# Kernel optimization log

Measured on AMD Instinct MI355X. Metric: run time of the kernel, lower is better.

## Reference

```python
import jax, jax.numpy as jnp
import numpy as np
from jax import lax

TAU = 2.0          # spikingjelly LIFNode default tau
VTH = 1.0          # v_threshold
ALPHA = 2.0        # ATan surrogate alpha (grad only; fwd is heaviside)
N_WIN = (2, 4, 4)
TOPK = 4
HEADS = 8
EPS = 1e-5


@jax.custom_vjp
def spike(x):
    return (x >= 0).astype(x.dtype)

def _spike_fwd(x):
    return (x >= 0).astype(x.dtype), x

def _spike_bwd(x, g):
    sg = (ALPHA / 2.0) / (1.0 + (jnp.pi / 2.0 * ALPHA * x) ** 2)
    return (g * sg,)

spike.defvjp(_spike_fwd, _spike_bwd)


def lif(x_seq):
    # multi-step LIF, v_reset=None (soft reset), decay_input=True, detach_reset
    def step(v, x):
        v = v + (x - v) / TAU
        s = spike(v - VTH)
        v = v - lax.stop_gradient(s) * VTH
        return v, s
    v0 = jnp.zeros_like(x_seq[0])
    _, s_seq = lax.scan(step, v0, x_seq)
    return s_seq


def bn3d(x, g, b):
    # track_running_stats=False -> always batch stats; step_mode 'm' folds T into batch.
    # x: [T,B,C,Lt,Lh,Lw]; normalize per-channel over (T,B,Lt,Lh,Lw)
    ax = (0, 1, 3, 4, 5)
    m = x.mean(ax, keepdims=True)
    v = x.var(ax, keepdims=True)
    sh = (1, 1, -1, 1, 1, 1)
    return g.reshape(sh) * (x - m) * lax.rsqrt(v + EPS) + b.reshape(sh)


def bra(x, wqkv, bqkv, lepe_w, wo, bo):
    # Bi-level routing attention over 3D windows. x: [N, Lt, Lh, Lw, C]
    N, Lt, Lh, Lw, C = x.shape
    nt, nh, nw = N_WIN
    rt, rh, rw = Lt // nt, Lh // nh, Lw // nw
    R, P = nt * nh * nw, rt * rh * rw
    Dh = C // HEADS

    qkv = x @ wqkv + bqkv                       # [N,Lt,Lh,Lw,3C]
    q, k, v = jnp.split(qkv, 3, axis=-1)

    def to_reg(t):  # -> [N, R, P, C]
        t = t.reshape(N, nt, rt, nh, rh, nw, rw, C)
        return t.transpose(0, 1, 3, 5, 2, 4, 6, 7).reshape(N, R, P, C)

    def from_reg(t):  # [N,R,P,C] -> [N,Lt,Lh,Lw,C]
        t = t.reshape(N, nt, nh, nw, rt, rh, rw, C)
        return t.transpose(0, 1, 4, 2, 5, 3, 6, 7).reshape(N, Lt, Lh, Lw, C)

    qr, kr, vr = to_reg(q), to_reg(k), to_reg(v)

    # coarse routing: region means, top-k region selection
    a_r = jnp.einsum('nrc,nsc->nrs', qr.mean(2), kr.mean(2))   # [N,R,R]
    _, idx = lax.top_k(a_r, TOPK)                               # [N,R,TOPK]

    # gather selected regions' k,v: [N,R,TOPK,P,C] -> [N,R,TOPK*P,H,Dh]
    kg = jax.vmap(lambda a, i: a[i])(kr, idx)
    vg = jax.vmap(lambda a, i: a[i])(vr, idx)
    kg = kg.reshape(N, R, TOPK * P, HEADS, Dh)
    vg = vg.reshape(N, R, TOPK * P, HEADS, Dh)
    qh = qr.reshape(N, R, P, HEADS, Dh)

    logits = jnp.einsum('nrphd,nrkhd->nrhpk', qh * (Dh ** -0.5), kg)
    attn = jax.nn.softmax(logits, axis=-1)
    out = jnp.einsum('nrhpk,nrkhd->nrphd', attn, vg).reshape(N, R, P, C)
    out = from_reg(out)

    # LEPE: depthwise 3x3x3 conv on v
    v_ncdhw = v.transpose(0, 4, 1, 2, 3)
    lepe = lax.conv_general_dilated(
        v_ncdhw, lepe_w, (1, 1, 1), 'SAME', feature_group_count=C,
        dimension_numbers=('NCDHW', 'OIDHW', 'NCDHW'))
    out = out + lepe.transpose(0, 2, 3, 4, 1)

    return out @ wo + bo


def setup_inputs() -> dict:
    key = jax.random.key(0)
    ks = jax.random.split(key, 8)
    T, B, C, Lt, Lh, Lw = 2, 1, 256, 8, 32, 32
    inp = {
        'x': jax.random.normal(ks[0], (T, B, C, Lt, Lh, Lw), jnp.float32),
        'bn1_g': jnp.ones((C,), jnp.float32),
        'bn1_b': jnp.zeros((C,), jnp.float32),
        'wqkv': jax.random.normal(ks[1], (C, 3 * C), jnp.float32) * (C ** -0.5),
        'bqkv': jnp.zeros((3 * C,), jnp.float32),
        'lepe_w': jax.random.normal(ks[2], (C, 1, 3, 3, 3), jnp.float32) * 0.1,
        'wo': jax.random.normal(ks[3], (C, C), jnp.float32) * (C ** -0.5),
        'bo': jnp.zeros((C,), jnp.float32),
        'bn2_g': jnp.ones((C,), jnp.float32),
        'bn2_b': jnp.zeros((C,), jnp.float32),
        'ffn_w1': jax.random.normal(ks[4], (C, 4 * C), jnp.float32) * (C ** -0.5),
        'ffn_b1': jnp.zeros((4 * C,), jnp.float32),
        'ffn_w2': jax.random.normal(ks[5], (4 * C, C), jnp.float32) * ((4 * C) ** -0.5),
        'ffn_b2': jnp.zeros((C,), jnp.float32),
        'scale': jnp.ones((1,), jnp.float32) * 0.5,
    }
    return inp


def reference(x, bn1_g, bn1_b, wqkv, bqkv, lepe_w, wo, bo,
              bn2_g, bn2_b, ffn_w1, ffn_b1, ffn_w2, ffn_b2, scale):
    T, B, C, Lt, Lh, Lw = x.shape

    # --- attention branch ---
    s1 = lif(bn3d(x, bn1_g, bn1_b))                       # [T,B,C,Lt,Lh,Lw]
    sa = s1.transpose(0, 1, 3, 4, 5, 2).reshape(T * B, Lt, Lh, Lw, C)
    a = bra(sa, wqkv, bqkv, lepe_w, wo, bo)
    a = a.reshape(T, B, Lt, Lh, Lw, C).transpose(0, 1, 5, 2, 3, 4)
    x = x + a * scale

    # --- FFN branch (1x1x1 conv = channel GEMM) ---
    s2 = lif(bn3d(x, bn2_g, bn2_b))
    h = jax.nn.gelu(jnp.einsum('tbcdhw,cf->tbfdhw', s2, ffn_w1)
                    + ffn_b1.reshape(1, 1, -1, 1, 1, 1), approximate=False)
    f = (jnp.einsum('tbfdhw,fc->tbcdhw', h, ffn_w2)
         + ffn_b2.reshape(1, 1, -1, 1, 1, 1))
    return x + f * scale
```

## Files before the change

kernel.cpp:

```cpp
#include <hip/hip_runtime.h>
#include <math.h>

#define CC 256
#define LL 8192
#define RR 32
#define PPP 256
#define NTOP 4
#define TOKS 16384
#define TBLK (TOKS * 32)

typedef unsigned short u16;
typedef __attribute__((ext_vector_type(8))) short short8;
typedef __attribute__((ext_vector_type(8))) unsigned short u16x8;
typedef __attribute__((ext_vector_type(4))) float f32x4;
typedef __attribute__((ext_vector_type(4))) unsigned short u16x4;

#if defined(__has_builtin)
#if __has_builtin(__builtin_amdgcn_exp2f)
#define EXP2(x) __builtin_amdgcn_exp2f(x)
#endif
#endif
#ifndef EXP2
#define EXP2(x) exp2f(x)
#endif

__device__ inline u16 f2bf(float f) {
  unsigned int b = __float_as_uint(f);
  unsigned int r = (b + 0x7FFFu + ((b >> 16) & 1u)) >> 16;
  return (u16)r;
}
__device__ inline float bf2f(u16 x) { return __uint_as_float(((unsigned int)x) << 16); }

__global__ __launch_bounds__(256) void k_bnstats(const float* __restrict__ x,
                                                 float* __restrict__ mean,
                                                 float* __restrict__ istd) {
  int c = blockIdx.x, tid = threadIdx.x;
  float s = 0.f, sq = 0.f;
  for (int i = tid; i < 2 * LL / 4; i += 256) {
    int t = i >> 11, l4 = (i & 2047) * 4;
    float4 v = *(const float4*)&x[(size_t)(t * CC + c) * LL + l4];
    s += (v.x + v.y) + (v.z + v.w);
    sq += (v.x * v.x + v.y * v.y) + (v.z * v.z + v.w * v.w);
  }
  __shared__ float rs[256], rq[256];
  rs[tid] = s; rq[tid] = sq;
  __syncthreads();
  for (int off = 128; off > 0; off >>= 1) {
    if (tid < off) { rs[tid] += rs[tid + off]; rq[tid] += rq[tid + off]; }
    __syncthreads();
  }
  if (tid == 0) {
    float m = rs[0] * (1.f / (2 * LL));
    float var = rq[0] * (1.f / (2 * LL)) - m * m;
    mean[c] = m;
    istd[c] = rsqrtf(var + 1e-5f);
  }
}

__global__ __launch_bounds__(128) void k_bnfin(const float* __restrict__ psum,
                                               const float* __restrict__ psq,
                                               float* __restrict__ mean,
                                               float* __restrict__ istd) {
  int c = blockIdx.x;
  int tid = threadIdx.x;
  __shared__ float rs[128], rq[128];
  rs[tid] = psum[c * 128 + tid];
  rq[tid] = psq[c * 128 + tid];
  __syncthreads();
  for (int off = 64; off > 0; off >>= 1) {
    if (tid < off) { rs[tid] += rs[tid + off]; rq[tid] += rq[tid + off]; }
    __syncthreads();
  }
  if (tid == 0) {
    float m = rs[0] * (1.f / 16384.f);
    float var = rq[0] * (1.f / 16384.f) - m * m;
    mean[c] = m;
    istd[c] = rsqrtf(var + 1e-5f);
  }
}

__global__ __launch_bounds__(256) void k_lifT(const float* __restrict__ xin,
                                              const float* __restrict__ mean,
                                              const float* __restrict__ istd,
                                              const float* __restrict__ g,
                                              const float* __restrict__ b,
                                              u16* __restrict__ actT) {
  __shared__ float t0[32][33], t1[32][33];
  int l0 = blockIdx.x * 32, c0 = blockIdx.y * 32;
  int tx = threadIdx.x & 31, ty = threadIdx.x >> 5;
  for (int i = 0; i < 32; i += 8) {
    int c = c0 + ty + i;
    float m = mean[c], is = istd[c], gg = g[c], bb = b[c];
    float x0 = xin[(size_t)c * LL + l0 + tx];
    float x1 = xin[(size_t)(CC + c) * LL + l0 + tx];
    float y0 = gg * (x0 - m) * is + bb;
    float y1 = gg * (x1 - m) * is + bb;
    float v = y0 * 0.5f;
    float s0 = (v >= 1.f) ? 1.f : 0.f;
    v -= s0;
    v += (y1 - v) * 0.5f;
    float s1 = (v >= 1.f) ? 1.f : 0.f;
    t0[ty + i][tx] = s0;
    t1[ty + i][tx] = s1;
  }
  __syncthreads();
  size_t kb = (size_t)(c0 >> 5) * TBLK;
  for (int i = 0; i < 32; i += 8) {
    int l = l0 + ty + i;
    actT[kb + (size_t)l * 32 + tx] = f2bf(t0[tx][ty + i]);
    actT[kb + (size_t)(LL + l) * 32 + tx] = f2bf(t1[tx][ty + i]);
  }
}

__device__ inline void tr_tile(const float* __restrict__ in, u16* __restrict__ out,
                               int C, int c0, int r0) {
  __shared__ float t[32][33];
  int tx = threadIdx.x & 31, ty = threadIdx.x >> 5;
  for (int i = 0; i < 32; i += 8)
    t[ty + i][tx] = in[(size_t)(r0 + ty + i) * C + c0 + tx];
  __syncthreads();
  size_t kb = (size_t)(r0 >> 5) * C * 32;
  for (int i = 0; i < 32; i += 8)
    out[kb + (size_t)(c0 + ty + i) * 32 + tx] = f2bf(t[tx][ty + i]);
}

__global__ __launch_bounds__(256) void k_trall(const float* __restrict__ wqkv,
                                               const float* __restrict__ w1,
                                               const float* __restrict__ w2,
                                               const float* __restrict__ wo,
                                               const float* __restrict__ lep,
                                               u16* __restrict__ wqkvT, u16* __restrict__ w1T,
                                               u16* __restrict__ w2T, u16* __restrict__ woT,
                                               float* __restrict__ wTlep) {
  int b = blockIdx.x;
  if (b < 192) {
    tr_tile(wqkv, wqkvT, 768, (b % 24) * 32, (b / 24) * 32);
  } else if (b < 448) {
    int i = b - 192;
    tr_tile(w1, w1T, 1024, (i % 32) * 32, (i / 32) * 32);
  } else if (b < 704) {
    int i = b - 448;
    tr_tile(w2, w2T, 256, (i % 8) * 32, (i / 8) * 32);
  } else if (b < 768) {
    int i = b - 704;
    tr_tile(wo, woT, 256, (i % 8) * 32, (i / 8) * 32);
  } else {
    int c = threadIdx.x;
    for (int tap = 0; tap < 27; ++tap) wTlep[tap * 256 + c] = lep[c * 27 + tap];
  }
}

template<int MR, int NR, int KTOT>
__device__ inline void mfma_core_w(const u16* __restrict__ A0, int sAb,
                                   const u16* __restrict__ B0, int sBb,
                                   int wr, int wc, f32x4 acc[MR][NR]) {
  int lane = threadIdx.x & 63;
  int u = lane & 15;
  int g8 = (lane >> 4) * 8;
  const u16* Ap = A0 + (wr * MR * 16 + u) * 32 + g8;
  const u16* Bp = B0 + (wc * NR * 16 + u) * 32 + g8;
  constexpr int NKB = KTOT >> 5;
  short8 aA[MR], bA[NR], aB[MR], bB[NR];
#pragma unroll
  for (int i = 0; i < MR; ++i) aA[i] = *(const short8*)(Ap + i * 512);
#pragma unroll
  for (int j = 0; j < NR; ++j) bA[j] = *(const short8*)(Bp + j * 512);
#pragma unroll
  for (int kb = 0; kb < NKB; kb += 2) {
    if (kb + 1 < NKB) {
#pragma unroll
      for (int i = 0; i < MR; ++i) aB[i] = *(const short8*)(Ap + (size_t)(kb + 1) * sAb + i * 512);
#pragma unroll
      for (int j = 0; j < NR; ++j) bB[j] = *(const short8*)(Bp + (size_t)(kb + 1) * sBb + j * 512);
    }
#pragma unroll
    for (int i = 0; i < MR; ++i)
#pragma unroll
      for (int j = 0; j < NR; ++j)
        acc[i][j] = __builtin_amdgcn_mfma_f32_16x16x32_bf16(aA[i], bA[j], acc[i][j], 0, 0, 0);
    if (kb + 2 < NKB) {
#pragma unroll
      for (int i = 0; i < MR; ++i) aA[i] = *(const short8*)(Ap + (size_t)(kb + 2) * sAb + i * 512);
#pragma unroll
      for (int j = 0; j < NR; ++j) bA[j] = *(const short8*)(Bp + (size_t)(kb + 2) * sBb + j * 512);
    }
    if (kb + 1 < NKB) {
#pragma unroll
      for (int i = 0; i < MR; ++i)
#pragma unroll
        for (int j = 0; j < NR; ++j)
          acc[i][j] = __builtin_amdgcn_mfma_f32_16x16x32_bf16(aB[i], bB[j], acc[i][j], 0, 0, 0);
    }
  }
}

__global__ __launch_bounds__(256) void k_gqkv(const u16* __restrict__ spkT, const u16* __restrict__ wT,
                                              const float* __restrict__ bias,
                                              u16* __restrict__ qh, u16* __restrict__ kh,
                                              u16* __restrict__ vt, u16* __restrict__ vtok) {
  f32x4 acc[4][4] = {};
  int m0 = blockIdx.x * 128, n0 = blockIdx.y * 128;
  int w = threadIdx.x >> 6;
  mfma_core_w<4, 4, 256>(spkT + (size_t)m0 * 32, TBLK, wT + (size_t)n0 * 32, 768 * 32,
                         w >> 1, w & 1, acc);
  int lane = threadIdx.x & 63;
  int wr = w >> 1, wc = w & 1;
  int u = lane & 15;
  const float QSC = 0.255034865f;
#pragma unroll
  for (int i = 0; i < 4; ++i) {
    int token0 = m0 + wr * 64 + i * 16 + (lane >> 4) * 4;
    int l = token0 & (LL - 1), nb = token0 >> 13;
    int lt = l >> 10, lh = (l >> 5) & 31, lw = l & 31;
    int r = ((lt >> 2) * 4 + (lh >> 3)) * 4 + (lw >> 3);
    int p0 = ((lt & 3) * 8 + (lh & 7)) * 8 + (lw & 7);
    int nr = nb * RR + r;
#pragma unroll
    for (int j = 0; j < 4; ++j) {
      int ch = n0 + wc * 64 + j * 16 + u;
      int which = ch >> 8, c = ch & 255;
      int hh = c >> 5, dh = c & 31;
      size_t hb = ((size_t)nr * 8 + hh) * 8192;
      float bb = bias[ch];
      if (which == 0) {
#pragma unroll
        for (int reg = 0; reg < 4; ++reg)
          qh[hb + (p0 + reg) * 32 + dh] = f2bf((acc[i][j][reg] + bb) * QSC);
      } else if (which == 1) {
#pragma unroll
        for (int reg = 0; reg < 4; ++reg)
          kh[hb + (p0 + reg) * 32 + dh] = f2bf(acc[i][j][reg] + bb);
      } else {
        u16x4 pk;
#pragma unroll
        for (int reg = 0; reg < 4; ++reg) {
          u16 vb = f2bf(acc[i][j][reg] + bb);
          pk[reg] = vb;
          vtok[(size_t)(token0 + reg) * CC + c] = vb;
        }
        *(u16x4*)&vt[hb + dh * 256 + p0] = pk;
      }
    }
  }
}

__global__ __launch_bounds__(256) void k_means(const u16* __restrict__ qh, const u16* __restrict__ kh,
                                               float* __restrict__ qm, float* __restrict__ km) {
  int nrh = blockIdx.x;
  int nr = nrh >> 3, h = nrh & 7;
  int tid = threadIdx.x;
  int dh = tid & 31, pg = tid >> 5;
  size_t base = (size_t)nrh * 8192;
  float sq = 0.f, sk = 0.f;
  for (int p = pg * 32; p < pg * 32 + 32; ++p) {
    sq += bf2f(qh[base + p * 32 + dh]);
    sk += bf2f(kh[base + p * 32 + dh]);
  }
  __shared__ float rq[256], rk[256];
  rq[tid] = sq; rk[tid] = sk;
  __syncthreads();
  if (pg == 0) {
#pragma unroll
    for (int g = 1; g < 8; ++g) { sq += rq[g * 32 + dh]; sk += rk[g * 32 + dh]; }
    qm[nr * 256 + h * 32 + dh] = sq * (1.f / 256);
    km[nr * 256 + h * 32 + dh] = sk * (1.f / 256);
  }
}

__global__ __launch_bounds__(256) void k_route(const float* __restrict__ qm,
                                               const float* __restrict__ km,
                                               int* __restrict__ idx) {
  int nr = blockIdx.x;
  int n = nr >> 5;
  int tid = threadIdx.x;
  int s = tid >> 3, cg = tid & 7;
  const float* qrow = qm + nr * CC;
  const float* krow = km + (n * RR + s) * CC;
  float sum = 0.f;
  for (int c = cg * 32; c < cg * 32 + 32; ++c) sum += qrow[c] * krow[c];
  sum += __shfl_xor(sum, 1);
  sum += __shfl_xor(sum, 2);
  sum += __shfl_xor(sum, 4);
  __shared__ float ar[32];
  if (cg == 0) ar[s] = sum;
  __syncthreads();
  if (tid == 0) {
    for (int t = 0; t < NTOP; ++t) {
      float best = -1e30f; int bi = 0;
      for (int ss = 0; ss < 32; ++ss)
        if (ar[ss] > best) { best = ar[ss]; bi = ss; }
      ar[bi] = -1e30f;
      idx[nr * NTOP + t] = bi;
    }
  }
}

__global__ __launch_bounds__(256) void k_attn_mfma(const u16* __restrict__ qh,
                                                   const u16* __restrict__ kh,
                                                   const u16* __restrict__ vt,
                                                   const int* __restrict__ idx,
                                                   u16* __restrict__ oreg) {
  int h = blockIdx.x, r = blockIdx.y, n = blockIdx.z;
  int nr = n * RR + r;
  int lane = threadIdx.x & 63;
  int w = threadIdx.x >> 6;
  int u = lane & 15, g = lane >> 4;
  int swz = (u >> 1) & 3;
  __shared__ __align__(16) unsigned pl[4096];
  unsigned* plw = &pl[w * 1024];

  const u16* qb = qh + ((size_t)nr * 8 + h) * 8192;
  int q0 = w * 64;
  short8 qf[4];
#pragma unroll
  for (int f = 0; f < 4; ++f)
    qf[f] = *(const short8*)(qb + (size_t)(q0 + f * 16 + u) * 32 + g * 8);

  f32x4 accO[2][4] = {};
  float lsum[4] = {0.f, 0.f, 0.f, 0.f};
  const int* idxp = &idx[nr * NTOP];

  for (int ri = 0; ri < NTOP; ++ri) {
    int reg = idxp[ri];
    size_t rb = ((size_t)(n * RR + reg) * 8 + h) * 8192;
#pragma unroll 2
    for (int t = 0; t < 8; ++t) {
      int pb = t * 32;
      short8 kf0 = *(const short8*)(kh + rb + (size_t)(pb + u) * 32 + g * 8);
      short8 kf1 = *(const short8*)(kh + rb + (size_t)(pb + 16 + u) * 32 + g * 8);
      short8 vf0 = *(const short8*)(vt + rb + (size_t)u * 256 + pb + g * 8);
      short8 vf1 = *(const short8*)(vt + rb + (size_t)(16 + u) * 256 + pb + g * 8);

      f32x4 s0[4], s1[4];
      __builtin_amdgcn_s_setprio(1);
#pragma unroll
      for (int nf = 0; nf < 4; ++nf) {
        s0[nf] = __builtin_amdgcn_mfma_f32_16x16x32_bf16(kf0, qf[nf], (f32x4){0.f, 0.f, 0.f, 0.f}, 0, 0, 0);
        s1[nf] = __builtin_amdgcn_mfma_f32_16x16x32_bf16(kf1, qf[nf], (f32x4){0.f, 0.f, 0.f, 0.f}, 0, 0, 0);
      }
      __builtin_amdgcn_s_setprio(0);
#pragma unroll
      for (int nf = 0; nf < 4; ++nf) {
#pragma unroll
        for (int mf = 0; mf < 2; ++mf) {
          f32x4 sv = mf ? s1[nf] : s0[nf];
          float p0 = EXP2(sv[0]);
          float p1 = EXP2(sv[1]);
          float p2 = EXP2(sv[2]);
          float p3 = EXP2(sv[3]);
          lsum[nf] += (p0 + p1) + (p2 + p3);
          unsigned wA, wB;
          asm("v_cvt_pk_bf16_f32 %0, %1, %2" : "=v"(wA) : "v"(p0), "v"(p1));
          asm("v_cvt_pk_bf16_f32 %0, %1, %2" : "=v"(wB) : "v"(p2), "v"(p3));
          int bidx = (mf * 2 + (g >> 1)) ^ swz;
          *(uint2*)&plw[nf * 256 + u * 16 + bidx * 4 + (g & 1) * 2] = make_uint2(wA, wB);
        }
      }
      __builtin_amdgcn_s_setprio(1);
#pragma unroll
      for (int nf = 0; nf < 4; ++nf) {
        short8 pf = *(const short8*)&plw[nf * 256 + u * 16 + ((g ^ swz) << 2)];
        accO[0][nf] = __builtin_amdgcn_mfma_f32_16x16x32_bf16(vf0, pf, accO[0][nf], 0, 0, 0);
        accO[1][nf] = __builtin_amdgcn_mfma_f32_16x16x32_bf16(vf1, pf, accO[1][nf], 0, 0, 0);
      }
      __builtin_amdgcn_s_setprio(0);
    }
  }

#pragma unroll
  for (int nf = 0; nf < 4; ++nf) {
    lsum[nf] += __shfl_xor(lsum[nf], 16);
    lsum[nf] += __shfl_xor(lsum[nf], 32);
    float inv = 1.f / lsum[nf];
    int q = q0 + nf * 16 + u;
    int z = (((r >> 4) & 1) << 2) | ((q >> 6) & 3);
    int y = (((r >> 2) & 3) << 3) | ((q >> 3) & 7);
    int xx = ((r & 3) << 3) | (q & 7);
    int l = (z << 10) | (y << 5) | xx;
    u16* ob = &oreg[((size_t)(n * LL + l)) * CC + h * 32];
#pragma unroll
    for (int mf = 0; mf < 2; ++mf) {
      f32x4 o = mf ? accO[1][nf] : accO[0][nf];
      float a0 = o[0] * inv, a1 = o[1] * inv, a2 = o[2] * inv, a3 = o[3] * inv;
      unsigned w0, w1;
      asm("v_cvt_pk_bf16_f32 %0, %1, %2" : "=v"(w0) : "v"(a0), "v"(a1));
      asm("v_cvt_pk_bf16_f32 %0, %1, %2" : "=v"(w1) : "v"(a2), "v"(a3));
      *(uint2*)&ob[mf * 16 + g * 4] = make_uint2(w0, w1);
    }
  }
}

__global__ __launch_bounds__(256) void k_lepe(const u16* __restrict__ oreg,
                                              const u16* __restrict__ vtok,
                                              const float* __restrict__ wT,
                                              u16* __restrict__ otok) {
  int vox = threadIdx.x >> 6;
  int b = blockIdx.x * 4 + vox;
  int l = b & (LL - 1);
  int lt = l >> 10, lh = (l >> 5) & 31, lw = l & 31;
  int c4 = (threadIdx.x & 63) * 4;
  const u16* vb = vtok + (size_t)b * CC + c4;
  float lx = 0.f, ly = 0.f, lz = 0.f, lww = 0.f;
#pragma unroll
  for (int dz = -1; dz <= 1; ++dz) {
#pragma unroll
    for (int dy = -1; dy <= 1; ++dy) {
#pragma unroll
      for (int dx = -1; dx <= 1; ++dx) {
        int z = lt + dz, y = lh + dy, xx = lw + dx;
        if (z >= 0 && z < 8 && y >= 0 && y < 32 && xx >= 0 && xx < 32) {
          int tap = ((dz + 1) * 3 + (dy + 1)) * 3 + (dx + 1);
          long off = (long)(dz * 1024 + dy * 32 + dx) * CC;
          float4 w4 = *(const float4*)&wT[tap * 256 + c4];
          u16x4 v4 = *(const u16x4*)&vb[off];
          lx = fmaf(w4.x, bf2f(v4[0]), lx);
          ly = fmaf(w4.y, bf2f(v4[1]), ly);
          lz = fmaf(w4.z, bf2f(v4[2]), lz);
          lww = fmaf(w4.w, bf2f(v4[3]), lww);
        }
      }
    }
  }
  u16x4 a4 = *(const u16x4*)&oreg[(size_t)b * CC + c4];
  size_t oaddr = (size_t)(c4 >> 5) * TBLK + (size_t)b * 32 + (c4 & 31);
  *(u16x4*)&otok[oaddr] =
      (u16x4){f2bf(bf2f(a4[0]) + lx), f2bf(bf2f(a4[1]) + ly),
              f2bf(bf2f(a4[2]) + lz), f2bf(bf2f(a4[3]) + lww)};
}

__global__ __launch_bounds__(256) void k_gffn(const u16* __restrict__ sT, const u16* __restrict__ w1T,
                                              const u16* __restrict__ w2T,
                                              const float* __restrict__ b1, const float* __restrict__ b2,
                                              const float* __restrict__ scale, float* __restrict__ out) {
  __shared__ __align__(16) u16 hl[4][32][40];
  int m0 = blockIdx.x * 32;
  int w = threadIdx.x >> 6, lane = threadIdx.x & 63;
  int u = lane & 15, g = lane >> 4;
  int g8 = g * 8;
  f32x4 acc2[4][4] = {};

  const u16* ApS = sT + (size_t)(m0 + u) * 32 + g8;
  const u16* Ap2 = w2T + (size_t)(w * 64 + u) * 32 + g8;

  for (int hc = 0; hc < 8; ++hc) {
    f32x4 acc1[2][2] = {};
    const u16* Bp1 = w1T + (size_t)(hc * 128 + w * 32 + u) * 32 + g8;
#pragma unroll
    for (int kb = 0; kb < 8; ++kb) {
      short8 a0 = *(const short8*)(ApS + (size_t)kb * TBLK);
      short8 a1 = *(const short8*)(ApS + (size_t)kb * TBLK + 512);
      short8 b0 = *(const short8*)(Bp1 + (size_t)kb * (1024 * 32));
      short8 bq = *(const short8*)(Bp1 + (size_t)kb * (1024 * 32) + 512);
      acc1[0][0] = __builtin_amdgcn_mfma_f32_16x16x32_bf16(a0, b0, acc1[0][0], 0, 0, 0);
      acc1[0][1] = __builtin_amdgcn_mfma_f32_16x16x32_bf16(a0, bq, acc1[0][1], 0, 0, 0);
      acc1[1][0] = __builtin_amdgcn_mfma_f32_16x16x32_bf16(a1, b0, acc1[1][0], 0, 0, 0);
      acc1[1][1] = __builtin_amdgcn_mfma_f32_16x16x32_bf16(a1, bq, acc1[1][1], 0, 0, 0);
    }
    __syncthreads();
#pragma unroll
    for (int i = 0; i < 2; ++i) {
#pragma unroll
      for (int reg = 0; reg < 4; ++reg) {
        int tokl = i * 16 + g * 4 + reg;
#pragma unroll
        for (int j = 0; j < 2; ++j) {
          int hh2 = j * 16 + u;
          float z = acc1[i][j][reg] + b1[hc * 128 + w * 32 + hh2];
          float z2 = z * z;
          float ea = z * fmaf(z2, 0.1029431f, 2.3022078f);
          float t = EXP2(ea);
          float th = (t - 1.f) * __builtin_amdgcn_rcpf(t + 1.f);
          float hz = 0.5f * z;
          hl[w][tokl][hh2] = f2bf(fmaf(hz, th, hz));
        }
      }
    }
    __syncthreads();
#pragma unroll
    for (int kb2 = 0; kb2 < 4; ++kb2) {
      const u16* a2 = Ap2 + (size_t)(hc * 4 + kb2) * (256 * 32);
      short8 af[4], bf2[2];
#pragma unroll
      for (int i = 0; i < 4; ++i) af[i] = *(const short8*)(a2 + i * 512);
#pragma unroll
      for (int j = 0; j < 2; ++j) bf2[j] = *(const short8*)&hl[kb2][j * 16 + u][g8];
#pragma unroll
      for (int i = 0; i < 4; ++i)
#pragma unroll
        for (int j = 0; j < 2; ++j)
          acc2[i][j] = __builtin_amdgcn_mfma_f32_16x16x32_bf16(af[i], bf2[j], acc2[i][j], 0, 0, 0);
    }
  }

  float sc = scale[0];
#pragma unroll
  for (int i = 0; i < 4; ++i) {
#pragma unroll
    for (int reg = 0; reg < 4; ++reg) {
      int ch = w * 64 + i * 16 + g * 4 + reg;
      float bb = b2[ch];
#pragma unroll
      for (int j = 0; j < 2; ++j) {
        int token = m0 + j * 16 + u;
        int t = token >> 13, l = token & (LL - 1);
        size_t oi = ((size_t)t * CC + ch) * LL + l;
        out[oi] += (acc2[i][j][reg] + bb) * sc;
      }
    }
  }
}

__global__ __launch_bounds__(256) void k_gwo(const u16* __restrict__ woT, const u16* __restrict__ atok,
                                             const float* __restrict__ bias, const float* __restrict__ xin,
                                             const float* __restrict__ scale, float* __restrict__ out,
                                             float* __restrict__ psum, float* __restrict__ psq) {
  __shared__ f32x4 red[2][2][4][64];
  __shared__ float lsum[2][32], lsq[2][32];
  f32x4 acc[2][4] = {};
  int n0 = blockIdx.x * 128, m0 = blockIdx.y * 32;
  int w = threadIdx.x >> 6, lane = threadIdx.x & 63;
  int kh2 = w >> 1, wc = w & 1;
  mfma_core_w<2, 4, 128>(woT + (size_t)m0 * 32 + (size_t)kh2 * 4 * (256 * 32), 256 * 32,
                         atok + (size_t)n0 * 32 + (size_t)kh2 * 4 * TBLK, TBLK,
                         0, wc, acc);
  if (w >= 2) {
#pragma unroll
    for (int i = 0; i < 2; ++i)
#pragma unroll
      for (int j = 0; j < 4; ++j)
        red[w - 2][i][j][lane] = acc[i][j];
  }
  __syncthreads();
  if (w < 2) {
    int g = lane >> 4;
    float sc = scale[0];
#pragma unroll
    for (int i = 0; i < 2; ++i)
#pragma unroll
      for (int j = 0; j < 4; ++j)
        acc[i][j] += red[w][i][j][lane];
#pragma unroll
    for (int i = 0; i < 2; ++i) {
#pragma unroll
      for (int reg = 0; reg < 4; ++reg) {
        int ch = m0 + i * 16 + g * 4 + reg;
        float bb = bias[ch];
        float s = 0.f, q = 0.f;
#pragma unroll
        for (int j = 0; j < 4; ++j) {
          int token = n0 + wc * 64 + j * 16 + (lane & 15);
          int t = token >> 13, l = token & (LL - 1);
          size_t oi = ((size_t)t * CC + ch) * LL + l;
          float v = xin[oi] + (acc[i][j][reg] + bb) * sc;
          out[oi] = v;
          s += v; q += v * v;
        }
        s += __shfl_xor(s, 1); q += __shfl_xor(q, 1);
        s += __shfl_xor(s, 2); q += __shfl_xor(q, 2);
        s += __shfl_xor(s, 4); q += __shfl_xor(q, 4);
        s += __shfl_xor(s, 8); q += __shfl_xor(q, 8);
        if ((lane & 15) == 0) {
          lsum[wc][i * 16 + g * 4 + reg] = s;
          lsq[wc][i * 16 + g * 4 + reg] = q;
        }
      }
    }
  }
  __syncthreads();
  int tid = threadIdx.x;
  if (tid < 32) {
    psum[(m0 + tid) * 128 + blockIdx.x] = lsum[0][tid] + lsum[1][tid];
    psq[(m0 + tid) * 128 + blockIdx.x] = lsq[0][tid] + lsq[1][tid];
  }
}

extern "C" void kernel_launch(void* const* d_in, const int* in_sizes, int n_in,
                              void* d_out, int out_size, void* d_ws, size_t ws_size,
                              hipStream_t stream) {
  const float* x      = (const float*)d_in[0];
  const float* bn1_g  = (const float*)d_in[1];
  const float* bn1_b  = (const float*)d_in[2];
  const float* wqkv   = (const float*)d_in[3];
  const float* bqkv   = (const float*)d_in[4];
  const float* lepe_w = (const float*)d_in[5];
  const float* wo_w   = (const float*)d_in[6];
  const float* bo     = (const float*)d_in[7];
  const float* bn2_g  = (const float*)d_in[8];
  const float* bn2_b  = (const float*)d_in[9];
  const float* ffn_w1 = (const float*)d_in[10];
  const float* ffn_b1 = (const float*)d_in[11];
  const float* ffn_w2 = (const float*)d_in[12];
  const float* ffn_b2 = (const float*)d_in[13];
  const float* scale  = (const float*)d_in[14];
  float* out = (float*)d_out;

  float* ws    = (float*)d_ws;
  u16*   actT  = (u16*)(ws + 4194304);
  u16*   qhead = (u16*)(ws + 6291456);
  u16*   khead = (u16*)(ws + 8388608);
  u16*   vthead= (u16*)(ws + 10485760);
  u16*   vtok  = (u16*)(ws + 12582912);
  u16*   oreg  = (u16*)(ws + 16777216);
  u16*   wqkvT = (u16*)(ws + 20971520);
  u16*   w1T   = (u16*)(ws + 21069824);
  u16*   w2T   = (u16*)(ws + 21200896);
  u16*   woT   = (u16*)(ws + 21331968);
  float* sm    = ws + 21364736;
  float* mean1 = sm;
  float* istd1 = sm + 256;
  float* mean2 = sm + 512;
  float* istd2 = sm + 768;
  float* qm    = sm + 1024;
  float* km    = sm + 1024 + 16384;
  int*   idxb  = (int*)(sm + 1024 + 32768);
  float* wTlep = sm + 1024 + 32768 + 256;
  float* psum  = sm + 1024 + 32768 + 256 + 6912;
  float* psq   = psum + 32768;

  k_trall<<<769, 256, 0, stream>>>(wqkv, ffn_w1, ffn_w2, wo_w, lepe_w,
                                   wqkvT, w1T, w2T, woT, wTlep);

  k_bnstats<<<256, 256, 0, stream>>>(x, mean1, istd1);
  k_lifT<<<dim3(256, 8), 256, 0, stream>>>(x, mean1, istd1, bn1_g, bn1_b, actT);
  k_gqkv<<<dim3(128, 6), 256, 0, stream>>>(actT, wqkvT, bqkv, qhead, khead, vthead, vtok);
  k_means<<<512, 256, 0, stream>>>(qhead, khead, qm, km);
  k_route<<<64, 256, 0, stream>>>(qm, km, idxb);
  k_attn_mfma<<<dim3(8, RR, 2), 256, 0, stream>>>(qhead, khead, vthead, idxb, oreg);
  k_lepe<<<4096, 256, 0, stream>>>(oreg, vtok, wTlep, actT);
  k_gwo<<<dim3(128, 8), 256, 0, stream>>>(woT, actT, bo, x, scale, out, psum, psq);

  k_bnfin<<<256, 128, 0, stream>>>(psum, psq, mean2, istd2);
  k_lifT<<<dim3(256, 8), 256, 0, stream>>>(out, mean2, istd2, bn2_g, bn2_b, actT);
  k_gffn<<<512, 256, 0, stream>>>(actT, w1T, w2T, ffn_b1, ffn_b2, scale, out);
}
```

Before: 189.3 us.

## Double-buffer GELU hidden tile in FFN kernel to overlap GEMM1 and GEMM2

Software-pipelines the fused FFN kernel by double-buffering the shared-memory hidden-activation tile. Each iteration now computes GEMM1 for the next hidden chunk and GEMM2 for the current chunk, then runs GELU on the next chunk, so only one barrier per chunk is needed instead of two. This aims to cut synchronisation stalls and let the MFMA work of both GEMMs interleave. In exchange it doubles the LDS buffer, fully unrolls the chunk loop, and raises register pressure.

```diff
diff --git a/kernel.cpp b/kernel.cpp
--- a/kernel.cpp
+++ b/kernel.cpp
@@ -428,11 +428,61 @@
               f2bf(bf2f(a4[2]) + lz), f2bf(bf2f(a4[3]) + lww)};
 }
 
+#define GEMM1(hcv, acc1) { \
+    const u16* Bp1 = w1T + (size_t)((hcv) * 128 + w * 32 + u) * 32 + g8; \
+    _Pragma("unroll") \
+    for (int kb = 0; kb < 8; ++kb) { \
+      short8 a0 = *(const short8*)(ApS + (size_t)kb * TBLK); \
+      short8 a1 = *(const short8*)(ApS + (size_t)kb * TBLK + 512); \
+      short8 b0 = *(const short8*)(Bp1 + (size_t)kb * (1024 * 32)); \
+      short8 bq = *(const short8*)(Bp1 + (size_t)kb * (1024 * 32) + 512); \
+      acc1[0][0] = __builtin_amdgcn_mfma_f32_16x16x32_bf16(a0, b0, acc1[0][0], 0, 0, 0); \
+      acc1[0][1] = __builtin_amdgcn_mfma_f32_16x16x32_bf16(a0, bq, acc1[0][1], 0, 0, 0); \
+      acc1[1][0] = __builtin_amdgcn_mfma_f32_16x16x32_bf16(a1, b0, acc1[1][0], 0, 0, 0); \
+      acc1[1][1] = __builtin_amdgcn_mfma_f32_16x16x32_bf16(a1, bq, acc1[1][1], 0, 0, 0); \
+    } }
+
+#define GELU_STORE(hcv, acc1, slab) { \
+    _Pragma("unroll") \
+    for (int i = 0; i < 2; ++i) { \
+      _Pragma("unroll") \
+      for (int reg = 0; reg < 4; ++reg) { \
+        int tokl = i * 16 + g * 4 + reg; \
+        _Pragma("unroll") \
+        for (int j = 0; j < 2; ++j) { \
+          int hh2 = j * 16 + u; \
+          float z = acc1[i][j][reg] + b1[(hcv) * 128 + w * 32 + hh2]; \
+          float z2 = z * z; \
+          float ea = z * fmaf(z2, 0.1029431f, 2.3022078f); \
+          float te = EXP2(ea); \
+          float th = (te - 1.f) * __builtin_amdgcn_rcpf(te + 1.f); \
+          float hz = 0.5f * z; \
+          hl[slab][w][tokl][hh2] = f2bf(fmaf(hz, th, hz)); \
+        } \
+      } \
+    } }
+
+#define GEMM2(hcv, slab) { \
+    _Pragma("unroll") \
+    for (int kb2 = 0; kb2 < 4; ++kb2) { \
+      const u16* a2 = Ap2 + (size_t)((hcv) * 4 + kb2) * (256 * 32); \
+      short8 af[4], bfv[2]; \
+      _Pragma("unroll") \
+      for (int i = 0; i < 4; ++i) af[i] = *(const short8*)(a2 + i * 512); \
+      _Pragma("unroll") \
+      for (int j = 0; j < 2; ++j) bfv[j] = *(const short8*)&hl[slab][kb2][j * 16 + u][g8]; \
+      _Pragma("unroll") \
+      for (int i = 0; i < 4; ++i) \
+        _Pragma("unroll") \
+        for (int j = 0; j < 2; ++j) \
+          acc2[i][j] = __builtin_amdgcn_mfma_f32_16x16x32_bf16(af[i], bfv[j], acc2[i][j], 0, 0, 0); \
+    } }
+
 __global__ __launch_bounds__(256) void k_gffn(const u16* __restrict__ sT, const u16* __restrict__ w1T,
                                               const u16* __restrict__ w2T,
                                               const float* __restrict__ b1, const float* __restrict__ b2,
                                               const float* __restrict__ scale, float* __restrict__ out) {
-  __shared__ __align__(16) u16 hl[4][32][40];
+  __shared__ __align__(16) u16 hl[2][4][32][40];
   int m0 = blockIdx.x * 32;
   int w = threadIdx.x >> 6, lane = threadIdx.x & 63;
   int u = lane & 15, g = lane >> 4;
@@ -442,55 +492,21 @@
   const u16* ApS = sT + (size_t)(m0 + u) * 32 + g8;
   const u16* Ap2 = w2T + (size_t)(w * 64 + u) * 32 + g8;
 
-  for (int hc = 0; hc < 8; ++hc) {
+  {
     f32x4 acc1[2][2] = {};
-    const u16* Bp1 = w1T + (size_t)(hc * 128 + w * 32 + u) * 32 + g8;
-#pragma unroll
-    for (int kb = 0; kb < 8; ++kb) {
-      short8 a0 = *(const short8*)(ApS + (size_t)kb * TBLK);
-      short8 a1 = *(const short8*)(ApS + (size_t)kb * TBLK + 512);
-      short8 b0 = *(const short8*)(Bp1 + (size_t)kb * (1024 * 32));
-      short8 bq = *(const short8*)(Bp1 + (size_t)kb * (1024 * 32) + 512);
-      acc1[0][0] = __builtin_amdgcn_mfma_f32_16x16x32_bf16(a0, b0, acc1[0][0], 0, 0, 0);
-      acc1[0][1] = __builtin_amdgcn_mfma_f32_16x16x32_bf16(a0, bq, acc1[0][1], 0, 0, 0);
-      acc1[1][0] = __builtin_amdgcn_mfma_f32_16x16x32_bf16(a1, b0, acc1[1][0], 0, 0, 0);
-      acc1[1][1] = __builtin_amdgcn_mfma_f32_16x16x32_bf16(a1, bq, acc1[1][1], 0, 0, 0);
-    }
+    GEMM1(0, acc1);
+    GELU_STORE(0, acc1, 0);
+  }
+  __syncthreads();
+#pragma unroll
+  for (int hc = 0; hc < 7; ++hc) {
+    f32x4 acc1[2][2] = {};
+    GEMM1(hc + 1, acc1);
+    GEMM2(hc, hc & 1);
+    GELU_STORE(hc + 1, acc1, (hc + 1) & 1);
     __syncthreads();
-#pragma unroll
-    for (int i = 0; i < 2; ++i) {
-#pragma unroll
-      for (int reg = 0; reg < 4; ++reg) {
-        int tokl = i * 16 + g * 4 + reg;
-#pragma unroll
-        for (int j = 0; j < 2; ++j) {
-          int hh2 = j * 16 + u;
-          float z = acc1[i][j][reg] + b1[hc * 128 + w * 32 + hh2];
-          float z2 = z * z;
-          float ea = z * fmaf(z2, 0.1029431f, 2.3022078f);
-          float t = EXP2(ea);
-          float th = (t - 1.f) * __builtin_amdgcn_rcpf(t + 1.f);
-          float hz = 0.5f * z;
-          hl[w][tokl][hh2] = f2bf(fmaf(hz, th, hz));
-        }
-      }
-    }
-    __syncthreads();
-#pragma unroll
-    for (int kb2 = 0; kb2 < 4; ++kb2) {
-      const u16* a2 = Ap2 + (size_t)(hc * 4 + kb2) * (256 * 32);
-      short8 af[4], bf2[2];
-#pragma unroll
-      for (int i = 0; i < 4; ++i) af[i] = *(const short8*)(a2 + i * 512);
-#pragma unroll
-      for (int j = 0; j < 2; ++j) bf2[j] = *(const short8*)&hl[kb2][j * 16 + u][g8];
-#pragma unroll
-      for (int i = 0; i < 4; ++i)
-#pragma unroll
-        for (int j = 0; j < 2; ++j)
-          acc2[i][j] = __builtin_amdgcn_mfma_f32_16x16x32_bf16(af[i], bf2[j], acc2[i][j], 0, 0, 0);
-    }
-  }
+  }
+  GEMM2(7, 1);
 
   float sc = scale[0];
 #pragma unroll
```

Result: slower. 194.2 us (+2.6%).
